# Kernel optimization log

Measured on AMD Instinct MI355X. Metric: run time of the kernel, lower is better.

Reference implementation:

```python
import jax, jax.numpy as jnp
import numpy as np

V, D, H, L, FF, T, B, W = 32000, 1024, 16, 8, 4096, 1024, 2, 256
HALF = FF // 2
HD = D // H
EPS = 1e-5


def layer_norm(x, g, b):
    mu = jnp.mean(x, axis=-1, keepdims=True)
    var = jnp.mean(jnp.square(x - mu), axis=-1, keepdims=True)
    return (x - mu) * jax.lax.rsqrt(var + EPS) * g + b


def setup_inputs() -> dict:
    key = jax.random.key(0)
    ks = jax.random.split(key, 12)
    s = 0.02
    nrm = lambda k, shape: jax.random.normal(k, shape, jnp.float32) * s
    idx = jax.random.randint(ks[0], (B, T), 0, V, dtype=jnp.int64)
    return {
        "idx": idx,
        "tok_emb": nrm(ks[1], (V, D)),
        "pos_emb": nrm(ks[2], (T, D)),
        "ln1_g": jnp.ones((L, D), jnp.float32),
        "ln1_b": jnp.zeros((L, D), jnp.float32),
        "qkv_w": nrm(ks[3], (L, 3 * D, D)),
        "out_w": nrm(ks[4], (L, D, D)),
        "ln2_g": jnp.ones((L, D), jnp.float32),
        "ln2_b": jnp.zeros((L, D), jnp.float32),
        "a_w1": nrm(ks[5], (L, HALF, D)),
        "a_w2": nrm(ks[6], (L, D, HALF)),
        "f_w1": nrm(ks[7], (L, HALF, D)),
        "f_w2": nrm(ks[8], (L, D, HALF)),
        "lnf_g": jnp.ones((D,), jnp.float32),
        "lnf_b": jnp.zeros((D,), jnp.float32),
        "head_w": nrm(ks[9], (V, D)),
    }


def _forward(idx, tok_emb, pos_emb, ln1_g, ln1_b, qkv_w, out_w, ln2_g, ln2_b,
             a_w1, a_w2, f_w1, f_w2, lnf_g, lnf_b, head_w):
    Bc, Tc = idx.shape
    x = tok_emb[idx] + pos_emb[:Tc]  # [B,T,D]
    # sliding-window causal band: attend to j in [i-W+1, i]
    i = jnp.arange(Tc)
    d = i[:, None] - i[None, :]
    mask = jnp.where((d >= 0) & (d < W), 0.0, -jnp.inf).astype(x.dtype)  # [T,T]
    scale = 1.0 / np.sqrt(HD)

    def block(x, p):
        l1g, l1b, qw, ow, l2g, l2b, aw1, aw2, fw1, fw2 = p
        h = layer_norm(x, l1g, l1b)
        qkv = (h @ qw.T).reshape(Bc, Tc, 3, H, HD)
        q, k, v = qkv[:, :, 0], qkv[:, :, 1], qkv[:, :, 2]  # [B,T,H,HD]
        attn = jnp.einsum('bqhd,bkhd->bhqk', q, k) * scale + mask
        attn = jax.nn.softmax(attn, axis=-1)
        o = jnp.einsum('bhqk,bkhd->bqhd', attn, v).reshape(Bc, Tc, D)
        x = x + o @ ow.T
        h2 = layer_norm(x, l2g, l2b)
        mlp = (jax.nn.gelu(h2 @ aw1.T, approximate=False) @ aw2.T
               + jax.nn.gelu(h2 @ fw1.T, approximate=False) @ fw2.T)
        return x + mlp, None

    x, _ = jax.lax.scan(block, x, (ln1_g, ln1_b, qkv_w, out_w, ln2_g, ln2_b,
                                   a_w1, a_w2, f_w1, f_w2))
    return layer_norm(x, lnf_g, lnf_b) @ head_w.T  # [B,T,V]


def reference(idx, tok_emb, pos_emb, ln1_g, ln1_b, qkv_w, out_w, ln2_g, ln2_b,
              a_w1, a_w2, f_w1, f_w2, lnf_g, lnf_b, head_w):
    return _forward(idx, tok_emb, pos_emb, ln1_g, ln1_b, qkv_w, out_w,
                    ln2_g, ln2_b, a_w1, a_w2, f_w1, f_w2, lnf_g, lnf_b, head_w)
```

## Files before the change

### kernel.cpp

```cpp
#include <hip/hip_runtime.h>

typedef __bf16 bf16x8 __attribute__((ext_vector_type(8)));
typedef __bf16 bf16x4 __attribute__((ext_vector_type(4)));
typedef float  f32x4  __attribute__((ext_vector_type(4)));
typedef unsigned int u32x4 __attribute__((ext_vector_type(4)));

#define MFMA16(a, b, c) __builtin_amdgcn_mfma_f32_16x16x32_bf16(a, b, c, 0, 0, 0)

__device__ __forceinline__ void gload_lds16(const void* g, void* l) {
  __builtin_amdgcn_global_load_lds(
      (const __attribute__((address_space(1))) void*)g,
      (__attribute__((address_space(3))) void*)l, 16, 0, 0);
}

__device__ __forceinline__ void waitvm(int vm) {
  if (vm == 6)      asm volatile("s_waitcnt vmcnt(6)" ::: "memory");
  else if (vm == 4) asm volatile("s_waitcnt vmcnt(4)" ::: "memory");
  else if (vm == 3) asm volatile("s_waitcnt vmcnt(3)" ::: "memory");
  else              asm volatile("s_waitcnt vmcnt(0)" ::: "memory");
}

__device__ __forceinline__ void cvt8(const float* __restrict__ s, __bf16* __restrict__ d) {
  f32x4 a = *(const f32x4*)s, b = *(const f32x4*)(s + 4);
  bf16x8 v;
  v[0] = (__bf16)a[0]; v[1] = (__bf16)a[1]; v[2] = (__bf16)a[2]; v[3] = (__bf16)a[3];
  v[4] = (__bf16)b[0]; v[5] = (__bf16)b[1]; v[6] = (__bf16)b[2]; v[7] = (__bf16)b[3];
  *(bf16x8*)d = v;
}

__global__ __launch_bounds__(256) void prepack_all(
    const float* __restrict__ qkv_w, const float* __restrict__ out_w,
    const float* __restrict__ a_w1, const float* __restrict__ f_w1,
    const float* __restrict__ a_w2, const float* __restrict__ f_w2,
    const float* __restrict__ head_w,
    __bf16* __restrict__ wq, __bf16* __restrict__ wo,
    __bf16* __restrict__ w1c, __bf16* __restrict__ w2c, __bf16* __restrict__ wh) {
  const int stride = gridDim.x * 256;
  for (int i = blockIdx.x * 256 + threadIdx.x; i < 16678912; i += stride) {
    if (i < 4194304) {
      if (i < 3145728) cvt8(qkv_w + ((size_t)i << 3), wq + ((size_t)i << 3));
      else {
        int j = i - 3145728;
        cvt8(out_w + ((size_t)j << 3), wo + ((size_t)j << 3));
      }
    } else if (i < 8388608) {
      int j = i - 4194304;
      int l = j >> 19, il = j & 524287;
      int k = (il & 127) * 8;
      int r = il >> 7;
      const float* s = (r < 2048)
          ? a_w1 + (size_t)l * 2097152 + ((size_t)r << 10) + k
          : f_w1 + (size_t)l * 2097152 + ((size_t)(r - 2048) << 10) + k;
      cvt8(s, w1c + ((size_t)j << 3));
    } else if (i < 12582912) {
      int j = i - 8388608;
      int l = j >> 19, il = j & 524287;
      int k = (il & 511) * 8;
      int r = il >> 9;
      const float* s = (k < 2048)
          ? a_w2 + (size_t)l * 2097152 + (size_t)r * 2048 + k
          : f_w2 + (size_t)l * 2097152 + (size_t)r * 2048 + (k - 2048);
      cvt8(s, w2c + ((size_t)j << 3));
    } else {
      int j = i - 12582912;
      cvt8(head_w + ((size_t)j << 3), wh + ((size_t)j << 3));
    }
  }
}

__global__ __launch_bounds__(256) void cvt_kernel(
    const float* __restrict__ s, __bf16* __restrict__ d, int n8) {
  int i = blockIdx.x * 256 + threadIdx.x;
  if (i >= n8) return;
  cvt8(s + ((size_t)i << 3), d + ((size_t)i << 3));
}

__global__ __launch_bounds__(256) void cat_w1_kernel(
    const float* __restrict__ a, const float* __restrict__ f, __bf16* __restrict__ d) {
  int i = blockIdx.x * 256 + threadIdx.x;
  int k = (i & 127) * 8;
  int r = i >> 7;
  const float* s = (r < 2048) ? a + ((size_t)r << 10) + k
                              : f + ((size_t)(r - 2048) << 10) + k;
  cvt8(s, d + ((size_t)i << 3));
}

__global__ __launch_bounds__(256) void cat_w2_kernel(
    const float* __restrict__ a, const float* __restrict__ f, __bf16* __restrict__ d) {
  int i = blockIdx.x * 256 + threadIdx.x;
  int k = (i & 511) * 8;
  int r = i >> 9;
  const float* s = (k < 2048) ? a + (size_t)r * 2048 + k
                              : f + (size_t)r * 2048 + (k - 2048);
  cvt8(s, d + ((size_t)i << 3));
}

__global__ __launch_bounds__(256) void embed_kernel(
    const int* __restrict__ idx, const float* __restrict__ te,
    const float* __restrict__ pe, float* __restrict__ x) {
  int m = blockIdx.x;
  int t = m & 1023;
  int tok = idx[m];
  int c = threadIdx.x * 4;
  f32x4 a = *(const f32x4*)(te + (size_t)tok * 1024 + c);
  f32x4 p = *(const f32x4*)(pe + (size_t)t * 1024 + c);
  *(f32x4*)(x + (size_t)m * 1024 + c) = a + p;
}

__global__ __launch_bounds__(256) void ln_kernel(
    const float* __restrict__ x, const float* __restrict__ g,
    const float* __restrict__ bb, __bf16* __restrict__ out) {
  int row = blockIdx.x, tid = threadIdx.x;
  int wid = tid >> 6, lane = tid & 63;
  f32x4 v = *(const f32x4*)(x + (size_t)row * 1024 + tid * 4);
  float s = v[0] + v[1] + v[2] + v[3];
  #pragma unroll
  for (int off = 32; off >= 1; off >>= 1) s += __shfl_xor(s, off);
  __shared__ float red1[4], red2[4];
  if (lane == 0) red1[wid] = s;
  __syncthreads();
  float mu = (red1[0] + red1[1] + red1[2] + red1[3]) * (1.0f / 1024.0f);
  float d0 = v[0] - mu, d1 = v[1] - mu, d2 = v[2] - mu, d3 = v[3] - mu;
  float q = d0 * d0 + d1 * d1 + d2 * d2 + d3 * d3;
  #pragma unroll
  for (int off = 32; off >= 1; off >>= 1) q += __shfl_xor(q, off);
  if (lane == 0) red2[wid] = q;
  __syncthreads();
  float var = (red2[0] + red2[1] + red2[2] + red2[3]) * (1.0f / 1024.0f);
  float inv = rsqrtf(var + 1e-5f);
  f32x4 gg = *(const f32x4*)(g + tid * 4);
  f32x4 bv = *(const f32x4*)(bb + tid * 4);
  bf16x4 o4;
  o4[0] = (__bf16)(d0 * inv * gg[0] + bv[0]);
  o4[1] = (__bf16)(d1 * inv * gg[1] + bv[1]);
  o4[2] = (__bf16)(d2 * inv * gg[2] + bv[2]);
  o4[3] = (__bf16)(d3 * inv * gg[3] + bv[3]);
  *(bf16x4*)(out + (size_t)row * 1024 + tid * 4) = o4;
}

template <int EPI>
__global__ __launch_bounds__(512, 2) void gemm256(
    const __bf16* __restrict__ A, int lda,
    const __bf16* __restrict__ B, int ldb, int K,
    float* __restrict__ Cf, __bf16* __restrict__ Cb, int ldc, int nbx) {
  __shared__ __align__(16) __bf16 lds[49152];
  const int tid = threadIdx.x, lane = tid & 63, w = tid >> 6;
  const int l15 = lane & 15, l4 = lane >> 4;
  const int wr = w >> 2, wc = w & 3;

  int nwg = gridDim.x, id = blockIdx.x;
  int q = nwg >> 3, r = nwg & 7;
  int xcd = id & 7, pos = id >> 3;
  int nid = (xcd < r ? xcd * (q + 1) : r * (q + 1) + (xcd - r) * q) + pos;
  int row0 = (nid % nbx) * 256, col0 = (nid / nbx) * 256;

  const __bf16* ag = A + (size_t)row0 * lda;
  const __bf16* bg = B + (size_t)col0 * ldb;

  f32x4 acc[8][4];
  #pragma unroll
  for (int i = 0; i < 8; ++i)
    #pragma unroll
    for (int j = 0; j < 4; ++j) acc[i][j] = (f32x4){0.f, 0.f, 0.f, 0.f};

  int srow[2], scol[2];
  #pragma unroll
  for (int i = 0; i < 2; ++i) {
    int p = (w + i * 8) * 1024 + lane * 16;
    int row = p >> 6, ch = (p >> 4) & 3;
    srow[i] = row;
    scol[i] = (ch ^ ((row >> 1) & 3)) * 8;
  }
  const int fx = (((l4 << 4) ^ (((l15 >> 1) & 3) << 4)) >> 1);

  auto stageA = [&](int t, int c) {
    #pragma unroll
    for (int i = 0; i < 2; ++i)
      gload_lds16(ag + (size_t)srow[i] * lda + t * 32 + scol[i],
                  &lds[c * 16384 + (w + i * 8) * 512]);
  };
  auto stageB = [&](int t, int c) {
    #pragma unroll
    for (int i = 0; i < 2; ++i)
      gload_lds16(bg + (size_t)srow[i] * ldb + t * 32 + scol[i],
                  &lds[c * 16384 + 8192 + (w + i * 8) * 512]);
  };

  auto kgroup = [&](int t2, int c, int cn, int vm, bool stg) {
    if (stg) stageA(t2, cn);
    waitvm(vm);
    __builtin_amdgcn_sched_barrier(0);
    __builtin_amdgcn_s_barrier();
    __builtin_amdgcn_sched_barrier(0);
    const int cb = c * 16384;
    bf16x8 bfr[4], af[4];
    #pragma unroll
    for (int ni = 0; ni < 4; ++ni)
      bfr[ni] = *(const bf16x8*)&lds[cb + 8192 + (wc * 64 + ni * 16 + l15) * 32 + fx];
    #pragma unroll
    for (int mi = 0; mi < 4; ++mi)
      af[mi] = *(const bf16x8*)&lds[cb + (wr * 128 + mi * 16 + l15) * 32 + fx];
    __builtin_amdgcn_s_setprio(1);
    #pragma unroll
    for (int mi = 0; mi < 4; ++mi)
      #pragma unroll
      for (int ni = 0; ni < 4; ++ni)
        acc[mi][ni] = MFMA16(af[mi], bfr[ni], acc[mi][ni]);
    __builtin_amdgcn_s_setprio(0);
    #pragma unroll
    for (int mi = 0; mi < 4; ++mi)
      af[mi] = *(const bf16x8*)&lds[cb + (wr * 128 + (mi + 4) * 16 + l15) * 32 + fx];
    if (stg) stageB(t2, cn);
    __builtin_amdgcn_s_setprio(1);
    #pragma unroll
    for (int mi = 0; mi < 4; ++mi)
      #pragma unroll
      for (int ni = 0; ni < 4; ++ni)
        acc[mi + 4][ni] = MFMA16(af[mi], bfr[ni], acc[mi + 4][ni]);
    __builtin_amdgcn_s_setprio(0);
    __builtin_amdgcn_sched_barrier(0);
    __builtin_amdgcn_s_barrier();
    __builtin_amdgcn_sched_barrier(0);
  };

  const int NT = K >> 5;
  stageA(0, 0); stageB(0, 0);
  stageA(1, 1); stageB(1, 1);

  int c = 0;
  for (int t = 0; t < NT - 2; ++t) {
    int cn = c + 2; if (cn >= 3) cn -= 3;
    kgroup(t + 2, c, cn, 6, true);
    c = (c == 2) ? 0 : c + 1;
  }
  kgroup(0, c, 0, 4, false);
  c = (c == 2) ? 0 : c + 1;
  kgroup(0, c, 0, 0, false);

  #pragma unroll
  for (int mi = 0; mi < 8; ++mi)
    #pragma unroll
    for (int ni = 0; ni < 4; ++ni)
      #pragma unroll
      for (int rr = 0; rr < 4; ++rr) {
        int row = row0 + wr * 128 + mi * 16 + l4 * 4 + rr;
        int col = col0 + wc * 64 + ni * 16 + l15;
        float v = acc[mi][ni][rr];
        size_t off = (size_t)row * ldc + col;
        if (EPI == 0) {
          Cf[off] = v;
        } else if (EPI == 1) {
          Cb[off] = (__bf16)v;
        } else {
          float gv = 0.5f * v * (1.0f + erff(v * 0.70710678118654752f));
          Cb[off] = (__bf16)gv;
        }
      }
}

template <int BN, int EPI>
__global__ __launch_bounds__(256) void gemm_bf16(
    const __bf16* __restrict__ A, int lda,
    const __bf16* __restrict__ B, int ldb, int K,
    float* __restrict__ Cf, __bf16* __restrict__ Cb, int ldc,
    const float* __restrict__ resid, int nbx) {
  constexpr int ACCN = BN / 32;
  constexpr int LB = BN / 64;
  constexpr int L = 2 + LB;
  __shared__ __align__(16) __bf16 As[3 * 4096];
  __shared__ __align__(16) __bf16 Bs[3 * BN * 32];

  int nwg = gridDim.x, id = blockIdx.x;
  int q = nwg >> 3, r = nwg & 7;
  int xcd = id & 7, pos = id >> 3;
  int nid = (xcd < r ? xcd * (q + 1) : r * (q + 1) + (xcd - r) * q) + pos;
  int row0 = (nid % nbx) * 128;
  int col0 = (nid / nbx) * BN;

  const int tid = threadIdx.x, lane = tid & 63, wid = tid >> 6;
  const int l15 = lane & 15, l4 = lane >> 4;
  const int wr = wid >> 1, wc = wid & 1;
  const int fx = (((l4 << 4) ^ (((l15 >> 1) & 3) << 4)) >> 1);

  f32x4 acc[4][ACCN];
  #pragma unroll
  for (int i = 0; i < 4; ++i)
    #pragma unroll
    for (int j = 0; j < ACCN; ++j) acc[i][j] = (f32x4){0.f, 0.f, 0.f, 0.f};

  const __bf16* aptr = A + (size_t)row0 * lda;
  const __bf16* bptr = B + (size_t)col0 * ldb;

  auto stage = [&](int t, int p) {
    #pragma unroll
    for (int i = 0; i < 2; ++i) {
      int ch = tid + 256 * i;
      int rr = ch >> 2, kc = ch & 3;
      gload_lds16(aptr + (size_t)rr * lda + t * 32 + (kc ^ ((rr >> 1) & 3)) * 8,
                  &As[p * 4096 + ch * 8]);
    }
    #pragma unroll
    for (int i = 0; i < LB; ++i) {
      int ch = tid + 256 * i;
      int rr = ch >> 2, kc = ch & 3;
      gload_lds16(bptr + (size_t)rr * ldb + t * 32 + (kc ^ ((rr >> 1) & 3)) * 8,
                  &Bs[p * BN * 32 + ch * 8]);
    }
  };

  const int NT = K >> 5;
  stage(0, 0);
  stage(1, 1);
  int p = 0;
  for (int t = 0; t < NT; ++t) {
    bool stg = (t + 2 < NT);
    if (stg) {
      int ps = p + 2; if (ps >= 3) ps -= 3;
      stage(t + 2, ps);
    }
    waitvm(stg ? 2 * L : ((t + 1 < NT) ? L : 0));
    __builtin_amdgcn_sched_barrier(0);
    __builtin_amdgcn_s_barrier();
    __builtin_amdgcn_sched_barrier(0);
    bf16x8 af[4], bfr[ACCN];
    #pragma unroll
    for (int mi = 0; mi < 4; ++mi)
      af[mi] = *(const bf16x8*)&As[p * 4096 + (wr * 64 + mi * 16 + l15) * 32 + fx];
    #pragma unroll
    for (int ni = 0; ni < ACCN; ++ni)
      bfr[ni] = *(const bf16x8*)&Bs[p * BN * 32 + (wc * (BN / 2) + ni * 16 + l15) * 32 + fx];
    __builtin_amdgcn_s_setprio(1);
    #pragma unroll
    for (int mi = 0; mi < 4; ++mi)
      #pragma unroll
      for (int ni = 0; ni < ACCN; ++ni)
        acc[mi][ni] = MFMA16(af[mi], bfr[ni], acc[mi][ni]);
    __builtin_amdgcn_s_setprio(0);
    __builtin_amdgcn_sched_barrier(0);
    __builtin_amdgcn_s_barrier();
    __builtin_amdgcn_sched_barrier(0);
    p = (p == 2) ? 0 : p + 1;
  }

  #pragma unroll
  for (int mi = 0; mi < 4; ++mi)
    #pragma unroll
    for (int ni = 0; ni < ACCN; ++ni)
      #pragma unroll
      for (int rr = 0; rr < 4; ++rr) {
        int row = row0 + wr * 64 + mi * 16 + l4 * 4 + rr;
        int col = col0 + wc * (BN / 2) + ni * 16 + l15;
        float v = acc[mi][ni][rr];
        size_t off = (size_t)row * ldc + col;
        if (EPI == 0) {
          Cf[off] = v;
        } else if (EPI == 1) {
          Cb[off] = (__bf16)v;
        } else if (EPI == 2) {
          float gv = 0.5f * v * (1.0f + erff(v * 0.70710678118654752f));
          Cb[off] = (__bf16)gv;
        } else {
          Cf[off] = resid[off] + v;
        }
      }
}

__global__ __launch_bounds__(256) void attn_kernel(
    const __bf16* __restrict__ qkv, __bf16* __restrict__ o) {
  const int bid = blockIdx.x;
  const int qt = bid & 15, h = (bid >> 4) & 15, b = bid >> 8;
  const int qs = qt * 64;
  const int ntiles = (qt + 1 < 5) ? (qt + 1) : 5;
  const int kt0 = qt - (ntiles - 1);

  __shared__ __align__(16) __bf16 Qs[64][72];
  __shared__ __align__(16) __bf16 KVs[64][72];
  __shared__ __align__(16) __bf16 Ssm[64][328];
  __shared__ float rsum[64];

  const int tid = threadIdx.x;
  const int lane = tid & 63, wid = tid >> 6;
  const int l15 = lane & 15, l4 = lane >> 4;
  const size_t rs = 3072;
  const __bf16* qbase = qkv + ((size_t)(b * 1024 + qs)) * rs + h * 64;

  #pragma unroll
  for (int i = 0; i < 2; ++i) {
    int c = tid * 2 + i;
    int rr = c >> 3, dc = c & 7;
    *(u32x4*)&Qs[rr][dc * 8] = *(const u32x4*)(qbase + (size_t)rr * rs + dc * 8);
  }

  for (int it = 0; it < ntiles; ++it) {
    int kt = kt0 + it;
    const __bf16* kbase = qkv + ((size_t)(b * 1024 + kt * 64)) * rs + 1024 + h * 64;
    __syncthreads();
    #pragma unroll
    for (int i = 0; i < 2; ++i) {
      int c = tid * 2 + i;
      int rr = c >> 3, dc = c & 7;
      *(u32x4*)&KVs[rr][dc * 8] = *(const u32x4*)(kbase + (size_t)rr * rs + dc * 8);
    }
    __syncthreads();
    bf16x8 aq[2];
    #pragma unroll
    for (int kk = 0; kk < 2; ++kk)
      aq[kk] = *(const bf16x8*)&Qs[16 * wid + l15][kk * 32 + l4 * 8];
    #pragma unroll
    for (int n = 0; n < 4; ++n) {
      f32x4 c4 = (f32x4){0.f, 0.f, 0.f, 0.f};
      #pragma unroll
      for (int kk = 0; kk < 2; ++kk) {
        bf16x8 bk = *(const bf16x8*)&KVs[n * 16 + l15][kk * 32 + l4 * 8];
        c4 = MFMA16(aq[kk], bk, c4);
      }
      int kj = kt * 64 + n * 16 + l15;
      int colS = it * 64 + n * 16 + l15;
      #pragma unroll
      for (int rr = 0; rr < 4; ++rr) {
        int qi = qs + 16 * wid + l4 * 4 + rr;
        int d = qi - kj;
        float sv = c4[rr] * 0.125f;
        Ssm[16 * wid + l4 * 4 + rr][colS] =
            (d >= 0 && d < 256) ? (__bf16)sv : (__bf16)(-1e30f);
      }
    }
  }
  __syncthreads();

  const int nc = ntiles * 4;
  for (int ro = 0; ro < 4; ++ro) {
    int row = 16 * wid + ro * 4 + l4;
    float vals[20];
    #pragma unroll
    for (int i = 0; i < 20; ++i) vals[i] = -3e38f;
    #pragma unroll
    for (int i = 0; i < 20; ++i)
      if (i < nc) vals[i] = (float)Ssm[row][l15 + 16 * i];
    float m = vals[0];
    #pragma unroll
    for (int i = 1; i < 20; ++i) m = fmaxf(m, vals[i]);
    #pragma unroll
    for (int off = 8; off >= 1; off >>= 1) m = fmaxf(m, __shfl_xor(m, off));
    float s = 0.f;
    #pragma unroll
    for (int i = 0; i < 20; ++i)
      if (i < nc) {
        float pp = __expf(vals[i] - m);
        s += pp;
        Ssm[row][l15 + 16 * i] = (__bf16)pp;
      }
    #pragma unroll
    for (int off = 8; off >= 1; off >>= 1) s += __shfl_xor(s, off);
    if (l15 == 0) rsum[row] = s;
  }

  f32x4 oacc[4];
  #pragma unroll
  for (int n = 0; n < 4; ++n) oacc[n] = (f32x4){0.f, 0.f, 0.f, 0.f};

  for (int it = 0; it < ntiles; ++it) {
    int kt = kt0 + it;
    const __bf16* vbase = qkv + ((size_t)(b * 1024 + kt * 64)) * rs + 2048 + h * 64;
    __syncthreads();
    {
      int k0 = (tid >> 4) * 4, d0 = (tid & 15) * 4;
      bf16x4 vr[4];
      #pragma unroll
      for (int rr = 0; rr < 4; ++rr)
        vr[rr] = *(const bf16x4*)(vbase + (size_t)(k0 + rr) * rs + d0);
      #pragma unroll
      for (int j = 0; j < 4; ++j) {
        bf16x4 wv;
        #pragma unroll
        for (int rr = 0; rr < 4; ++rr) wv[rr] = vr[rr][j];
        *(bf16x4*)&KVs[d0 + j][k0] = wv;
      }
    }
    __syncthreads();
    #pragma unroll
    for (int kk = 0; kk < 2; ++kk) {
      bf16x8 ap = *(const bf16x8*)&Ssm[16 * wid + l15][it * 64 + kk * 32 + l4 * 8];
      #pragma unroll
      for (int n = 0; n < 4; ++n) {
        bf16x8 bv = *(const bf16x8*)&KVs[n * 16 + l15][kk * 32 + l4 * 8];
        oacc[n] = MFMA16(ap, bv, oacc[n]);
      }
    }
  }

  #pragma unroll
  for (int n = 0; n < 4; ++n)
    #pragma unroll
    for (int rr = 0; rr < 4; ++rr) {
      int qrow = 16 * wid + l4 * 4 + rr;
      float inv = 1.0f / rsum[qrow];
      size_t m = (size_t)(b * 1024 + qs + qrow);
      o[m * 1024 + h * 64 + n * 16 + l15] = (__bf16)(oacc[n][rr] * inv);
    }
}

extern "C" void kernel_launch(void* const* d_in, const int* in_sizes, int n_in,
                              void* d_out, int out_size, void* d_ws, size_t ws_size,
                              hipStream_t stream) {
  (void)in_sizes; (void)n_in; (void)out_size;
  const int*   idx     = (const int*)d_in[0];
  const float* tok_emb = (const float*)d_in[1];
  const float* pos_emb = (const float*)d_in[2];
  const float* ln1_g   = (const float*)d_in[3];
  const float* ln1_b   = (const float*)d_in[4];
  const float* qkv_w   = (const float*)d_in[5];
  const float* out_w   = (const float*)d_in[6];
  const float* ln2_g   = (const float*)d_in[7];
  const float* ln2_b   = (const float*)d_in[8];
  const float* a_w1    = (const float*)d_in[9];
  const float* a_w2    = (const float*)d_in[10];
  const float* f_w1    = (const float*)d_in[11];
  const float* f_w2    = (const float*)d_in[12];
  const float* lnf_g   = (const float*)d_in[13];
  const float* lnf_b   = (const float*)d_in[14];
  const float* head_w  = (const float*)d_in[15];
  float* out = (float*)d_out;

  char* ws = (char*)d_ws;
  float*  x    = (float*)(ws);
  __bf16* h    = (__bf16*)(ws + 8388608);
  __bf16* qkv  = (__bf16*)(ws + 12582912);
  __bf16* oatt = (__bf16*)(ws + 25165824);
  __bf16* gcat = (__bf16*)(ws + 29360128);

  const bool full = ws_size >= 313000000ull;

  __bf16 *wq, *wo, *w1c, *w2c, *wh;
  if (full) {
    wq  = (__bf16*)(ws + 46137344);
    wo  = (__bf16*)(ws + 96468992);
    w1c = (__bf16*)(ws + 113246208);
    w2c = (__bf16*)(ws + 180355072);
    wh  = (__bf16*)(ws + 247463936);
    prepack_all<<<2048, 256, 0, stream>>>(
        qkv_w, out_w, a_w1, f_w1, a_w2, f_w2, head_w, wq, wo, w1c, w2c, wh);
  } else {
    wq  = (__bf16*)(ws + 46137344);
    wo  = (__bf16*)(ws + 52428800);
    w1c = (__bf16*)(ws + 54525952);
    w2c = (__bf16*)(ws + 62914560);
    wh  = (__bf16*)(ws + 46137344);
  }

  embed_kernel<<<2048, 256, 0, stream>>>(idx, tok_emb, pos_emb, x);

  for (int l = 0; l < 8; ++l) {
    const __bf16 *wq_l, *wo_l, *w1_l, *w2_l;
    if (full) {
      wq_l = wq + (size_t)l * 3072 * 1024;
      wo_l = wo + (size_t)l * 1024 * 1024;
      w1_l = w1c + (size_t)l * 4096 * 1024;
      w2_l = w2c + (size_t)l * 1024 * 4096;
    } else {
      cvt_kernel<<<1536, 256, 0, stream>>>(qkv_w + (size_t)l * 3072 * 1024, wq, 393216);
      cvt_kernel<<<512, 256, 0, stream>>>(out_w + (size_t)l * 1024 * 1024, wo, 131072);
      cat_w1_kernel<<<2048, 256, 0, stream>>>(
          a_w1 + (size_t)l * 2048 * 1024, f_w1 + (size_t)l * 2048 * 1024, w1c);
      cat_w2_kernel<<<2048, 256, 0, stream>>>(
          a_w2 + (size_t)l * 1024 * 2048, f_w2 + (size_t)l * 1024 * 2048, w2c);
      wq_l = wq; wo_l = wo; w1_l = w1c; w2_l = w2c;
    }

    ln_kernel<<<2048, 256, 0, stream>>>(x, ln1_g + l * 1024, ln1_b + l * 1024, h);
    gemm_bf16<128, 1><<<16 * 24, 256, 0, stream>>>(
        h, 1024, wq_l, 1024, 1024, nullptr, qkv, 3072, nullptr, 16);
    attn_kernel<<<512, 256, 0, stream>>>(qkv, oatt);
    gemm_bf16<64, 3><<<16 * 16, 256, 0, stream>>>(
        oatt, 1024, wo_l, 1024, 1024, x, nullptr, 1024, x, 16);
    ln_kernel<<<2048, 256, 0, stream>>>(x, ln2_g + l * 1024, ln2_b + l * 1024, h);
    gemm_bf16<128, 2><<<16 * 32, 256, 0, stream>>>(
        h, 1024, w1_l, 1024, 1024, nullptr, gcat, 4096, nullptr, 16);
    gemm_bf16<64, 3><<<16 * 16, 256, 0, stream>>>(
        gcat, 4096, w2_l, 4096, 4096, x, nullptr, 1024, x, 16);
  }

  if (!full) {
    cvt_kernel<<<16000, 256, 0, stream>>>(head_w, wh, 4096000);
  }
  ln_kernel<<<2048, 256, 0, stream>>>(x, lnf_g, lnf_b, h);
  gemm256<0><<<8 * 125, 512, 0, stream>>>(
      h, 1024, wh, 1024, 1024, out, nullptr, 32000, 8);
}
```

Measured before the change: 1.926 ms.

## Load attention Q/K fragments straight to registers, flatten prepack grid

After: 1.937 ms. About the same (+0.5%).

```diff
diff --git a/kernel.cpp b/kernel.cpp
--- a/kernel.cpp
+++ b/kernel.cpp
@@ -35,36 +35,34 @@
     const float* __restrict__ head_w,
     __bf16* __restrict__ wq, __bf16* __restrict__ wo,
     __bf16* __restrict__ w1c, __bf16* __restrict__ w2c, __bf16* __restrict__ wh) {
-  const int stride = gridDim.x * 256;
-  for (int i = blockIdx.x * 256 + threadIdx.x; i < 16678912; i += stride) {
-    if (i < 4194304) {
-      if (i < 3145728) cvt8(qkv_w + ((size_t)i << 3), wq + ((size_t)i << 3));
-      else {
-        int j = i - 3145728;
-        cvt8(out_w + ((size_t)j << 3), wo + ((size_t)j << 3));
-      }
-    } else if (i < 8388608) {
-      int j = i - 4194304;
-      int l = j >> 19, il = j & 524287;
-      int k = (il & 127) * 8;
-      int r = il >> 7;
-      const float* s = (r < 2048)
-          ? a_w1 + (size_t)l * 2097152 + ((size_t)r << 10) + k
-          : f_w1 + (size_t)l * 2097152 + ((size_t)(r - 2048) << 10) + k;
-      cvt8(s, w1c + ((size_t)j << 3));
-    } else if (i < 12582912) {
-      int j = i - 8388608;
-      int l = j >> 19, il = j & 524287;
-      int k = (il & 511) * 8;
-      int r = il >> 9;
-      const float* s = (k < 2048)
-          ? a_w2 + (size_t)l * 2097152 + (size_t)r * 2048 + k
-          : f_w2 + (size_t)l * 2097152 + (size_t)r * 2048 + (k - 2048);
-      cvt8(s, w2c + ((size_t)j << 3));
-    } else {
-      int j = i - 12582912;
-      cvt8(head_w + ((size_t)j << 3), wh + ((size_t)j << 3));
-    }
+  int i = blockIdx.x * 256 + threadIdx.x;
+  if (i < 4194304) {
+    if (i < 3145728) cvt8(qkv_w + ((size_t)i << 3), wq + ((size_t)i << 3));
+    else {
+      int j = i - 3145728;
+      cvt8(out_w + ((size_t)j << 3), wo + ((size_t)j << 3));
+    }
+  } else if (i < 8388608) {
+    int j = i - 4194304;
+    int l = j >> 19, il = j & 524287;
+    int k = (il & 127) * 8;
+    int r = il >> 7;
+    const float* s = (r < 2048)
+        ? a_w1 + (size_t)l * 2097152 + ((size_t)r << 10) + k
+        : f_w1 + (size_t)l * 2097152 + ((size_t)(r - 2048) << 10) + k;
+    cvt8(s, w1c + ((size_t)j << 3));
+  } else if (i < 12582912) {
+    int j = i - 8388608;
+    int l = j >> 19, il = j & 524287;
+    int k = (il & 511) * 8;
+    int r = il >> 9;
+    const float* s = (k < 2048)
+        ? a_w2 + (size_t)l * 2097152 + (size_t)r * 2048 + k
+        : f_w2 + (size_t)l * 2097152 + (size_t)r * 2048 + (k - 2048);
+    cvt8(s, w2c + ((size_t)j << 3));
+  } else if (i < 16678912) {
+    int j = i - 12582912;
+    cvt8(head_w + ((size_t)j << 3), wh + ((size_t)j << 3));
   }
 }
 
@@ -373,8 +371,7 @@
   const int ntiles = (qt + 1 < 5) ? (qt + 1) : 5;
   const int kt0 = qt - (ntiles - 1);
 
-  __shared__ __align__(16) __bf16 Qs[64][72];
-  __shared__ __align__(16) __bf16 KVs[64][72];
+  __shared__ __align__(16) __bf16 Vt[64][72];
   __shared__ __align__(16) __bf16 Ssm[64][328];
   __shared__ float rsum[64];
 
@@ -382,38 +379,24 @@
   const int lane = tid & 63, wid = tid >> 6;
   const int l15 = lane & 15, l4 = lane >> 4;
   const size_t rs = 3072;
-  const __bf16* qbase = qkv + ((size_t)(b * 1024 + qs)) * rs + h * 64;
-
-  #pragma unroll
-  for (int i = 0; i < 2; ++i) {
-    int c = tid * 2 + i;
-    int rr = c >> 3, dc = c & 7;
-    *(u32x4*)&Qs[rr][dc * 8] = *(const u32x4*)(qbase + (size_t)rr * rs + dc * 8);
-  }
+
+  const __bf16* qrow =
+      qkv + ((size_t)(b * 1024 + qs + 16 * wid + l15)) * rs + h * 64;
+  bf16x8 aq[2];
+  aq[0] = *(const bf16x8*)(qrow + l4 * 8);
+  aq[1] = *(const bf16x8*)(qrow + 32 + l4 * 8);
 
   for (int it = 0; it < ntiles; ++it) {
     int kt = kt0 + it;
     const __bf16* kbase = qkv + ((size_t)(b * 1024 + kt * 64)) * rs + 1024 + h * 64;
-    __syncthreads();
-    #pragma unroll
-    for (int i = 0; i < 2; ++i) {
-      int c = tid * 2 + i;
-      int rr = c >> 3, dc = c & 7;
-      *(u32x4*)&KVs[rr][dc * 8] = *(const u32x4*)(kbase + (size_t)rr * rs + dc * 8);
-    }
-    __syncthreads();
-    bf16x8 aq[2];
-    #pragma unroll
-    for (int kk = 0; kk < 2; ++kk)
-      aq[kk] = *(const bf16x8*)&Qs[16 * wid + l15][kk * 32 + l4 * 8];
     #pragma unroll
     for (int n = 0; n < 4; ++n) {
+      const __bf16* krow = kbase + (size_t)(n * 16 + l15) * rs;
+      bf16x8 bk0 = *(const bf16x8*)(krow + l4 * 8);
+      bf16x8 bk1 = *(const bf16x8*)(krow + 32 + l4 * 8);
       f32x4 c4 = (f32x4){0.f, 0.f, 0.f, 0.f};
-      #pragma unroll
-      for (int kk = 0; kk < 2; ++kk) {
-        bf16x8 bk = *(const bf16x8*)&KVs[n * 16 + l15][kk * 32 + l4 * 8];
-        c4 = MFMA16(aq[kk], bk, c4);
-      }
+      c4 = MFMA16(aq[0], bk0, c4);
+      c4 = MFMA16(aq[1], bk1, c4);
       int kj = kt * 64 + n * 16 + l15;
       int colS = it * 64 + n * 16 + l15;
       #pragma unroll
@@ -426,7 +409,6 @@
       }
     }
   }
-  __syncthreads();
 
   const int nc = ntiles * 4;
   for (int ro = 0; ro < 4; ++ro) {
@@ -474,7 +456,7 @@
         bf16x4 wv;
         #pragma unroll
         for (int rr = 0; rr < 4; ++rr) wv[rr] = vr[rr][j];
-        *(bf16x4*)&KVs[d0 + j][k0] = wv;
+        *(bf16x4*)&Vt[d0 + j][k0] = wv;
       }
     }
     __syncthreads();
@@ -483,7 +465,7 @@
       bf16x8 ap = *(const bf16x8*)&Ssm[16 * wid + l15][it * 64 + kk * 32 + l4 * 8];
       #pragma unroll
       for (int n = 0; n < 4; ++n) {
-        bf16x8 bv = *(const bf16x8*)&KVs[n * 16 + l15][kk * 32 + l4 * 8];
+        bf16x8 bv = *(const bf16x8*)&Vt[n * 16 + l15][kk * 32 + l4 * 8];
         oacc[n] = MFMA16(ap, bv, oacc[n]);
       }
     }
@@ -493,9 +475,9 @@
   for (int n = 0; n < 4; ++n)
     #pragma unroll
     for (int rr = 0; rr < 4; ++rr) {
-      int qrow = 16 * wid + l4 * 4 + rr;
-      float inv = 1.0f / rsum[qrow];
-      size_t m = (size_t)(b * 1024 + qs + qrow);
+      int qrow2 = 16 * wid + l4 * 4 + rr;
+      float inv = 1.0f / rsum[qrow2];
+      size_t m = (size_t)(b * 1024 + qs + qrow2);
       o[m * 1024 + h * 64 + n * 16 + l15] = (__bf16)(oacc[n][rr] * inv);
     }
 }
@@ -538,7 +520,7 @@
     w1c = (__bf16*)(ws + 113246208);
     w2c = (__bf16*)(ws + 180355072);
     wh  = (__bf16*)(ws + 247463936);
-    prepack_all<<<2048, 256, 0, stream>>>(
+    prepack_all<<<65152, 256, 0, stream>>>(
         qkv_w, out_w, a_w1, f_w1, a_w2, f_w2, head_w, wq, wo, w1c, w2c, wh);
   } else {
     wq  = (__bf16*)(ws + 46137344);
```
